# Kernel tuning notes

Hardware: AMD Instinct MI355X
Metric: run time of the kernel (lower is better)

The kernel has to match this reference:

```python
import jax, jax.numpy as jnp
import numpy as np

RES = 192
VOXEL_LEN = 2.0 / (RES - 1)
AABB_LO, AABB_HI = -1.0, 1.0
SH_DIM = 9
UNIFORM = 0.5

_C0 = 0.28209479177387814
_C1 = 0.4886025119029199
_C2 = (1.0925484305920792, -1.0925484305920792, 0.31539156525252005,
       -1.0925484305920792, 0.5462742152960396)

_CORNERS = np.array([[-1, -1, -1], [-1, -1, 1], [-1, 1, -1], [-1, 1, 1],
                     [1, -1, -1], [1, -1, 1], [1, 1, -1], [1, 1, 1]], dtype=np.float32)


def _sh_basis(d):
    # degree-2 real spherical harmonics basis, [B, 9]
    x, y, z = d[..., 0], d[..., 1], d[..., 2]
    return jnp.stack([
        jnp.full_like(x, _C0),
        -_C1 * y, _C1 * z, -_C1 * x,
        _C2[0] * x * y, _C2[1] * y * z,
        _C2[2] * (2.0 * z * z - x * x - y * y),
        _C2[3] * x * z, _C2[4] * (x * x - y * y),
    ], axis=-1)


def _interp_weights(xyz):
    # trilinear weights matching get_interp_weights corner ordering, [..., 8]
    x, y, z = xyz[..., 0], xyz[..., 1], xyz[..., 2]
    return jnp.stack([
        (1 - x) * (1 - y) * (1 - z), (1 - x) * (1 - y) * z,
        (1 - x) * y * (1 - z), (1 - x) * y * z,
        x * (1 - y) * (1 - z), x * (1 - y) * z,
        x * y * (1 - z), x * y * z], axis=-1)


def setup_inputs() -> dict:
    key = jax.random.key(0)
    k1, k2, k3 = jax.random.split(key, 3)
    B = 1024
    # rays originating on a radius-3 sphere, pointing roughly at the aabb center
    rays_o = jax.random.normal(k1, (B, 3), dtype=jnp.float32)
    rays_o = 3.0 * rays_o / jnp.linalg.norm(rays_o, axis=-1, keepdims=True)
    rays_d = -rays_o / 3.0 + 0.08 * jax.random.normal(k2, (B, 3), dtype=jnp.float32)
    rays_d = rays_d / jnp.linalg.norm(rays_d, axis=-1, keepdims=True)
    grid_data = 0.1 * jax.random.normal(k3, (RES ** 3, 3 * SH_DIM + 1), dtype=jnp.float32)
    grid_idx = jnp.arange(RES ** 3, dtype=jnp.int32).reshape(RES, RES, RES)
    return {"rays_o": rays_o, "rays_d": rays_d, "grid_data": grid_data,
            "grid_idx": grid_idx, "n_samples": 400}


def reference(rays_o, rays_d, grid_data, grid_idx, n_samples):
    B = rays_o.shape[0]
    step = VOXEL_LEN
    # --- get_intersections (no-grad in original) ---
    op = (AABB_HI - rays_o) / rays_d
    on = (AABB_LO - rays_o) / rays_d
    t_in = jnp.max(jnp.minimum(op, on), axis=-1)   # [B]
    t_out = jnp.min(jnp.maximum(op, on), axis=-1)  # [B]
    w = jnp.linspace(0.0, 1.0, n_samples, dtype=rays_o.dtype)
    start = t_in + UNIFORM * step
    end = t_in + UNIFORM * step * n_samples
    intrs = start[:, None] * (1.0 - w) + end[:, None] * w   # [B, S]
    intrs = jax.lax.stop_gradient(jnp.minimum(intrs, t_out[:, None]))

    # --- get_intersection_ids: neighbor voxel gather coordinates ---
    pts = rays_o[:, None, :] + intrs[:, :, None] * rays_d[:, None, :]  # [B,S,3]
    offs = jnp.asarray(_CORNERS) * (VOXEL_LEN / 2)                      # [8,3]
    neigh = pts[:, :, None, :] + offs[None, None]                       # [B,S,8,3]
    ngc = jnp.floor(neigh / VOXEL_LEN + 1e-5)
    centers = jnp.clip((ngc + 0.5) * VOXEL_LEN,
                       AABB_LO + VOXEL_LEN / 2, AABB_HI - VOXEL_LEN / 2)
    ids = jnp.clip((ngc + RES / 2).astype(jnp.int32), 0, RES - 1)
    xyzs = (pts - centers[:, :, 0, :]) / VOXEL_LEN                      # [B,S,3]
    nidx = grid_idx[ids[..., 0], ids[..., 1], ids[..., 2]]              # [B,S,8]

    # --- gather + trilinear interpolation (weights are non-diff in original) ---
    nd = grid_data[nidx]                                                 # [B,S,8,28]
    weights = jax.lax.stop_gradient(_interp_weights(xyzs))              # [B,S,8]
    feat = jnp.einsum('bsec,bse->bsc', nd, weights)                      # [B,S,28]

    sigma = feat[..., -1]                                                # [B,S]
    sh = feat[..., :-1].reshape(B, -1, 3, SH_DIM)                        # [B,S,3,9]
    dirs = rays_d / jnp.linalg.norm(rays_d, axis=-1, keepdims=True)
    rgb = jnp.einsum('bsck,bk->bsc', sh, _sh_basis(dirs))                # [B,S,3]

    # --- volumetric_rendering (uses S-1 intervals) ---
    dists = jnp.diff(intrs, axis=1) * jnp.linalg.norm(rays_d, axis=-1, keepdims=True)
    alpha = 1.0 - jnp.exp(-jax.nn.relu(sigma[:, :-1]) * dists)           # [B,S-1]
    cum = jnp.concatenate([jnp.ones((B, 1), alpha.dtype),
                           jnp.cumprod(1.0 - alpha[:, :-1] + 1e-10, axis=-1)], axis=-1)
    abs_light = alpha * cum
    acc = abs_light.sum(-1)
    rgb_map = (abs_light[..., None] * jax.nn.sigmoid(rgb[:, :-1])).sum(axis=1)  # [B,3]
    depth = jax.lax.stop_gradient((abs_light * intrs[:, :-1]).sum(-1))
    rgb_map = rgb_map + (1.0 - acc[:, None])  # white background
    return rgb_map, alpha, depth
```

## Files before the change

kernel.cpp:

```cpp
#include <hip/hip_runtime.h>
#include <cstddef>


constexpr int   RES  = 192;
constexpr float VLEN = 2.0f / 191.0f;
constexpr int   SM1  = 399;
constexpr int   ROWB = 28 * 4;

__global__ __launch_bounds__(512) void nerf_render(
    const float* __restrict__ rays_o,
    const float* __restrict__ rays_d,
    const float* __restrict__ grid_data,
    float* __restrict__ out, int B)
{
  const int b    = blockIdx.x;
  const int tid  = threadIdx.x;
  const int wave = tid >> 6;
  const int lane = tid & 63;
  const int srel = lane >> 3;
  const int r    = lane & 7;

  __shared__ float s_alpha[SM1];
  __shared__ float s_rgb0[SM1];
  __shared__ float s_rgb1[SM1];
  __shared__ float s_rgb2[SM1];
  __shared__ int4  s_m0[SM1];
  __shared__ int4  s_m1[SM1];
  __shared__ float s_m2[SM1];
  __shared__ float s_bs[9];

  const float ox = rays_o[b*3+0], oy = rays_o[b*3+1], oz = rays_o[b*3+2];
  const float dx = rays_d[b*3+0], dy = rays_d[b*3+1], dz = rays_d[b*3+2];

  const float opx = (1.0f - ox)/dx, onx = (-1.0f - ox)/dx;
  const float opy = (1.0f - oy)/dy, ony = (-1.0f - oy)/dy;
  const float opz = (1.0f - oz)/dz, onz = (-1.0f - oz)/dz;
  const float t_in  = fmaxf(fmaxf(fminf(opx,onx), fminf(opy,ony)), fminf(opz,onz));
  const float t_out = fminf(fminf(fmaxf(opx,onx), fmaxf(opy,ony)), fmaxf(opz,onz));
  const float h = 0.5f * VLEN;
  const float dnorm = sqrtf(dx*dx + dy*dy + dz*dz);

  if (tid == 0) {
    const float inv = 1.0f / dnorm;
    const float x = dx*inv, y = dy*inv, z = dz*inv;
    s_bs[0] = 0.28209479177387814f;
    s_bs[1] = -0.4886025119029199f * y;
    s_bs[2] =  0.4886025119029199f * z;
    s_bs[3] = -0.4886025119029199f * x;
    s_bs[4] =  1.0925484305920792f * x*y;
    s_bs[5] = -1.0925484305920792f * y*z;
    s_bs[6] =  0.31539156525252005f * (2.0f*z*z - x*x - y*y);
    s_bs[7] = -1.0925484305920792f * x*z;
    s_bs[8] =  0.5462742152960396f * (x*x - y*y);
  }

  const float hv = 0.5f * VLEN;
  const float inv_vlen = 1.0f / VLEN;

  if (tid < SM1) {
    const int s = tid;
    const float t  = fminf(t_in + h*(float)(s+1), t_out);
    const float px = ox + t*dx, py = oy + t*dy, pz = oz + t*dz;

    const float nx0 = floorf((px - hv)*inv_vlen + 1e-5f);
    const float nx1 = floorf((px + hv)*inv_vlen + 1e-5f);
    const float ny0 = floorf((py - hv)*inv_vlen + 1e-5f);
    const float ny1 = floorf((py + hv)*inv_vlen + 1e-5f);
    const float nz0 = floorf((pz - hv)*inv_vlen + 1e-5f);
    const float nz1 = floorf((pz + hv)*inv_vlen + 1e-5f);

    const int ix0 = min(max((int)(nx0 + 96.0f), 0), RES-1);
    const int ix1 = min(max((int)(nx1 + 96.0f), 0), RES-1);
    const int iy0 = min(max((int)(ny0 + 96.0f), 0), RES-1);
    const int iy1 = min(max((int)(ny1 + 96.0f), 0), RES-1);
    const int iz0 = min(max((int)(nz0 + 96.0f), 0), RES-1);
    const int iz1 = min(max((int)(nz1 + 96.0f), 0), RES-1);

    const float cx = fminf(fmaxf((nx0 + 0.5f)*VLEN, -1.0f + hv), 1.0f - hv);
    const float cy = fminf(fmaxf((ny0 + 0.5f)*VLEN, -1.0f + hv), 1.0f - hv);
    const float cz = fminf(fmaxf((nz0 + 0.5f)*VLEN, -1.0f + hv), 1.0f - hv);
    const float fx = (px - cx)*inv_vlen, fy = (py - cy)*inv_vlen, fz = (pz - cz)*inv_vlen;

    const int x0 = ix0 * (RES*RES*ROWB), x1 = ix1 * (RES*RES*ROWB);
    const int y0 = iy0 * (RES*ROWB),     y1 = iy1 * (RES*ROWB);
    s_m0[s] = make_int4(x0 + y0, x0 + y1, x1 + y0, x1 + y1);
    s_m1[s] = make_int4(iz0 * ROWB, iz1 * ROWB,
                        __float_as_int(fx), __float_as_int(fy));
    s_m2[s] = fz;
  }
  __syncthreads();

  float c0[4], c1[4], c2[4], cs[4];
  #pragma unroll
  for (int j = 0; j < 4; ++j) {
    const int c = 4*r + j;
    float b0 = 0.0f, b1 = 0.0f, b2 = 0.0f, bsg = 0.0f;
    if (c < 9)       b0  = s_bs[c];
    else if (c < 18) b1  = s_bs[c - 9];
    else if (c < 27) b2  = s_bs[c - 18];
    else if (c == 27) bsg = 1.0f;
    c0[j] = b0; c1[j] = b1; c2[j] = b2; cs[j] = bsg;
  }

  float* out_rgb   = out;
  float* out_alpha = out + (size_t)B*3;
  float* out_depth = out + (size_t)B*3 + (size_t)B*SM1;

  const char* gbase = (const char*)grid_data + 16*min(r, 6);

  float4 va[2][8];
  int4   m1s[2];
  float  m2s[2];

  auto issue = [&](int p, int slot) {
    const int sc = min(p*64 + wave*8 + srel, SM1-1);
    const int4 a0 = s_m0[sc];
    const int4 a1 = s_m1[sc];
    m1s[slot] = a1;
    m2s[slot] = s_m2[sc];
    va[slot][0] = *reinterpret_cast<const float4*>(gbase + (a0.x + a1.x));
    va[slot][1] = *reinterpret_cast<const float4*>(gbase + (a0.x + a1.y));
    va[slot][2] = *reinterpret_cast<const float4*>(gbase + (a0.y + a1.x));
    va[slot][3] = *reinterpret_cast<const float4*>(gbase + (a0.y + a1.y));
    va[slot][4] = *reinterpret_cast<const float4*>(gbase + (a0.z + a1.x));
    va[slot][5] = *reinterpret_cast<const float4*>(gbase + (a0.z + a1.y));
    va[slot][6] = *reinterpret_cast<const float4*>(gbase + (a0.w + a1.x));
    va[slot][7] = *reinterpret_cast<const float4*>(gbase + (a0.w + a1.y));
  };

  auto consume = [&](int p, int slot) {
    const int s = p*64 + wave*8 + srel;
    if (s >= SM1) return;
    const float fx = __int_as_float(m1s[slot].z);
    const float fy = __int_as_float(m1s[slot].w);
    const float fz = m2s[slot];
    const float wx0 = 1.0f - fx, wy0 = 1.0f - fy, wz0 = 1.0f - fz;
    const float p00 = wx0*wy0, p01 = wx0*fy, p10 = fx*wy0, p11 = fx*fy;
    const float w[8] = { p00*wz0, p00*fz, p01*wz0, p01*fz,
                         p10*wz0, p10*fz, p11*wz0, p11*fz };
    float ax = 0.f, ay = 0.f, az = 0.f, aw = 0.f;
    #pragma unroll
    for (int e = 0; e < 8; ++e) {
      ax = fmaf(w[e], va[slot][e].x, ax);
      ay = fmaf(w[e], va[slot][e].y, ay);
      az = fmaf(w[e], va[slot][e].z, az);
      aw = fmaf(w[e], va[slot][e].w, aw);
    }
    float pr0 = ax*c0[0] + ay*c0[1] + az*c0[2] + aw*c0[3];
    float pr1 = ax*c1[0] + ay*c1[1] + az*c1[2] + aw*c1[3];
    float pr2 = ax*c2[0] + ay*c2[1] + az*c2[2] + aw*c2[3];
    float sg  = ax*cs[0] + ay*cs[1] + az*cs[2] + aw*cs[3];
    #pragma unroll
    for (int o = 1; o <= 4; o <<= 1) {
      pr0 += __shfl_xor(pr0, o, 64);
      pr1 += __shfl_xor(pr1, o, 64);
      pr2 += __shfl_xor(pr2, o, 64);
      sg  += __shfl_xor(sg,  o, 64);
    }
    if (r == 0) {
      const float t  = fminf(t_in + h*(float)(s+1), t_out);
      const float tn = fminf(t_in + h*(float)(s+2), t_out);
      const float dist = (tn - t) * dnorm;
      const float sig  = fmaxf(sg, 0.0f);
      s_alpha[s] = 1.0f - __expf(-sig * dist);
      s_rgb0[s] = 1.0f/(1.0f + __expf(-pr0));
      s_rgb1[s] = 1.0f/(1.0f + __expf(-pr1));
      s_rgb2[s] = 1.0f/(1.0f + __expf(-pr2));
    }
  };

  issue(0, 0);
  #pragma unroll
  for (int p = 0; p < 7; ++p) {
    if (p < 6) issue(p + 1, (p + 1) & 1);
    consume(p, p & 1);
  }
  __syncthreads();

  if (tid < SM1) out_alpha[(size_t)b*SM1 + tid] = s_alpha[tid];

  if (tid < 64) {
    const int ln = tid;
    const int s0 = ln * 7;
    float pr = 1.0f;
    #pragma unroll
    for (int i = 0; i < 7; ++i) {
      const int si = s0 + i;
      const float tt = (si < SM1) ? (1.0f - s_alpha[si] + 1e-10f) : 1.0f;
      pr *= tt;
    }
    float incl = pr;
    #pragma unroll
    for (int off = 1; off < 64; off <<= 1) {
      const float vv = __shfl_up(incl, off, 64);
      if (ln >= off) incl *= vv;
    }
    float cum = __shfl_up(incl, 1, 64);
    if (ln == 0) cum = 1.0f;

    float acc = 0.0f, r0 = 0.0f, r1 = 0.0f, r2 = 0.0f, dep = 0.0f;
    #pragma unroll
    for (int i = 0; i < 7; ++i) {
      const int si = s0 + i;
      if (si < SM1) {
        const float al = s_alpha[si];
        const float ab = al * cum;
        acc += ab;
        r0 = fmaf(ab, s_rgb0[si], r0);
        r1 = fmaf(ab, s_rgb1[si], r1);
        r2 = fmaf(ab, s_rgb2[si], r2);
        const float ti = fminf(t_in + h*(float)(si+1), t_out);
        dep = fmaf(ab, ti, dep);
        cum *= (1.0f - al + 1e-10f);
      }
    }
    #pragma unroll
    for (int off = 32; off; off >>= 1) {
      acc += __shfl_down(acc, off, 64);
      r0  += __shfl_down(r0,  off, 64);
      r1  += __shfl_down(r1,  off, 64);
      r2  += __shfl_down(r2,  off, 64);
      dep += __shfl_down(dep, off, 64);
    }
    if (ln == 0) {
      const float bg = 1.0f - acc;
      out_rgb[b*3+0] = r0 + bg;
      out_rgb[b*3+1] = r1 + bg;
      out_rgb[b*3+2] = r2 + bg;
      out_depth[b]   = dep;
    }
  }
}

extern "C" void kernel_launch(void* const* d_in, const int* in_sizes, int n_in,
                              void* d_out, int out_size, void* d_ws, size_t ws_size,
                              hipStream_t stream) {
  const float* rays_o    = (const float*)d_in[0];
  const float* rays_d    = (const float*)d_in[1];
  const float* grid_data = (const float*)d_in[2];
  const int B = in_sizes[0] / 3;
  nerf_render<<<dim3(B), dim3(512), 0, stream>>>(
      rays_o, rays_d, grid_data, (float*)d_out, B);
}
```

Before: 33.72 us.

## Halve block size to 256 threads and drop manual double-buffered gather pipeline

Blocks shrink from 512 to 256 threads with launch bounds targeting 5 blocks per CU. The setup and gather loops become strided so each wave handles more samples. The explicit two-slot register prefetch of grid corners is replaced by a plain loop that loads and consumes in the same iteration. The aim is lower register pressure and more resident waves to hide gather latency, at the cost of less software-managed overlap within each wave.

```diff
diff --git a/kernel.cpp b/kernel.cpp
--- a/kernel.cpp
+++ b/kernel.cpp
@@ -7,7 +7,7 @@
 constexpr int   SM1  = 399;
 constexpr int   ROWB = 28 * 4;
 
-__global__ __launch_bounds__(512) void nerf_render(
+__global__ __launch_bounds__(256, 5) void nerf_render(
     const float* __restrict__ rays_o,
     const float* __restrict__ rays_d,
     const float* __restrict__ grid_data,
@@ -57,8 +57,7 @@
   const float hv = 0.5f * VLEN;
   const float inv_vlen = 1.0f / VLEN;
 
-  if (tid < SM1) {
-    const int s = tid;
+  for (int s = tid; s < SM1; s += 256) {
     const float t  = fminf(t_in + h*(float)(s+1), t_out);
     const float px = ox + t*dx, py = oy + t*dy, pz = oz + t*dz;
 
@@ -102,82 +101,73 @@
     c0[j] = b0; c1[j] = b1; c2[j] = b2; cs[j] = bsg;
   }
 
+  const char* gbase = (const char*)grid_data + 16*min(r, 6);
+
+  for (int p = 0; p < 13; ++p) {
+    const int s = p*32 + wave*8 + srel;
+    if (s < SM1) {
+      const int4 a0 = s_m0[s];
+      const int4 a1 = s_m1[s];
+      const float fz = s_m2[s];
+
+      float4 va[8];
+      va[0] = *reinterpret_cast<const float4*>(gbase + (a0.x + a1.x));
+      va[1] = *reinterpret_cast<const float4*>(gbase + (a0.x + a1.y));
+      va[2] = *reinterpret_cast<const float4*>(gbase + (a0.y + a1.x));
+      va[3] = *reinterpret_cast<const float4*>(gbase + (a0.y + a1.y));
+      va[4] = *reinterpret_cast<const float4*>(gbase + (a0.z + a1.x));
+      va[5] = *reinterpret_cast<const float4*>(gbase + (a0.z + a1.y));
+      va[6] = *reinterpret_cast<const float4*>(gbase + (a0.w + a1.x));
+      va[7] = *reinterpret_cast<const float4*>(gbase + (a0.w + a1.y));
+
+      const float fx = __int_as_float(a1.z);
+      const float fy = __int_as_float(a1.w);
+      const float wx0 = 1.0f - fx, wy0 = 1.0f - fy, wz0 = 1.0f - fz;
+      const float p00 = wx0*wy0, p01 = wx0*fy, p10 = fx*wy0, p11 = fx*fy;
+      const float w[8] = { p00*wz0, p00*fz, p01*wz0, p01*fz,
+                           p10*wz0, p10*fz, p11*wz0, p11*fz };
+
+      float ax = 0.f, ay = 0.f, az = 0.f, aw = 0.f;
+      #pragma unroll
+      for (int e = 0; e < 8; ++e) {
+        ax = fmaf(w[e], va[e].x, ax);
+        ay = fmaf(w[e], va[e].y, ay);
+        az = fmaf(w[e], va[e].z, az);
+        aw = fmaf(w[e], va[e].w, aw);
+      }
+      float pr0 = ax*c0[0] + ay*c0[1] + az*c0[2] + aw*c0[3];
+      float pr1 = ax*c1[0] + ay*c1[1] + az*c1[2] + aw*c1[3];
+      float pr2 = ax*c2[0] + ay*c2[1] + az*c2[2] + aw*c2[3];
+      float sg  = ax*cs[0] + ay*cs[1] + az*cs[2] + aw*cs[3];
+
+      #pragma unroll
+      for (int o = 1; o <= 4; o <<= 1) {
+        pr0 += __shfl_xor(pr0, o, 64);
+        pr1 += __shfl_xor(pr1, o, 64);
+        pr2 += __shfl_xor(pr2, o, 64);
+        sg  += __shfl_xor(sg,  o, 64);
+      }
+
+      if (r == 0) {
+        const float t  = fminf(t_in + h*(float)(s+1), t_out);
+        const float tn = fminf(t_in + h*(float)(s+2), t_out);
+        const float dist = (tn - t) * dnorm;
+        const float sig  = fmaxf(sg, 0.0f);
+        s_alpha[s] = 1.0f - __expf(-sig * dist);
+        s_rgb0[s] = 1.0f/(1.0f + __expf(-pr0));
+        s_rgb1[s] = 1.0f/(1.0f + __expf(-pr1));
+        s_rgb2[s] = 1.0f/(1.0f + __expf(-pr2));
+      }
+    }
+  }
+  __syncthreads();
+
   float* out_rgb   = out;
   float* out_alpha = out + (size_t)B*3;
   float* out_depth = out + (size_t)B*3 + (size_t)B*SM1;
 
-  const char* gbase = (const char*)grid_data + 16*min(r, 6);
-
-  float4 va[2][8];
-  int4   m1s[2];
-  float  m2s[2];
-
-  auto issue = [&](int p, int slot) {
-    const int sc = min(p*64 + wave*8 + srel, SM1-1);
-    const int4 a0 = s_m0[sc];
-    const int4 a1 = s_m1[sc];
-    m1s[slot] = a1;
-    m2s[slot] = s_m2[sc];
-    va[slot][0] = *reinterpret_cast<const float4*>(gbase + (a0.x + a1.x));
-    va[slot][1] = *reinterpret_cast<const float4*>(gbase + (a0.x + a1.y));
-    va[slot][2] = *reinterpret_cast<const float4*>(gbase + (a0.y + a1.x));
-    va[slot][3] = *reinterpret_cast<const float4*>(gbase + (a0.y + a1.y));
-    va[slot][4] = *reinterpret_cast<const float4*>(gbase + (a0.z + a1.x));
-    va[slot][5] = *reinterpret_cast<const float4*>(gbase + (a0.z + a1.y));
-    va[slot][6] = *reinterpret_cast<const float4*>(gbase + (a0.w + a1.x));
-    va[slot][7] = *reinterpret_cast<const float4*>(gbase + (a0.w + a1.y));
-  };
-
-  auto consume = [&](int p, int slot) {
-    const int s = p*64 + wave*8 + srel;
-    if (s >= SM1) return;
-    const float fx = __int_as_float(m1s[slot].z);
-    const float fy = __int_as_float(m1s[slot].w);
-    const float fz = m2s[slot];
-    const float wx0 = 1.0f - fx, wy0 = 1.0f - fy, wz0 = 1.0f - fz;
-    const float p00 = wx0*wy0, p01 = wx0*fy, p10 = fx*wy0, p11 = fx*fy;
-    const float w[8] = { p00*wz0, p00*fz, p01*wz0, p01*fz,
-                         p10*wz0, p10*fz, p11*wz0, p11*fz };
-    float ax = 0.f, ay = 0.f, az = 0.f, aw = 0.f;
-    #pragma unroll
-    for (int e = 0; e < 8; ++e) {
-      ax = fmaf(w[e], va[slot][e].x, ax);
-      ay = fmaf(w[e], va[slot][e].y, ay);
-      az = fmaf(w[e], va[slot][e].z, az);
-      aw = fmaf(w[e], va[slot][e].w, aw);
-    }
-    float pr0 = ax*c0[0] + ay*c0[1] + az*c0[2] + aw*c0[3];
-    float pr1 = ax*c1[0] + ay*c1[1] + az*c1[2] + aw*c1[3];
-    float pr2 = ax*c2[0] + ay*c2[1] + az*c2[2] + aw*c2[3];
-    float sg  = ax*cs[0] + ay*cs[1] + az*cs[2] + aw*cs[3];
-    #pragma unroll
-    for (int o = 1; o <= 4; o <<= 1) {
-      pr0 += __shfl_xor(pr0, o, 64);
-      pr1 += __shfl_xor(pr1, o, 64);
-      pr2 += __shfl_xor(pr2, o, 64);
-      sg  += __shfl_xor(sg,  o, 64);
-    }
-    if (r == 0) {
-      const float t  = fminf(t_in + h*(float)(s+1), t_out);
-      const float tn = fminf(t_in + h*(float)(s+2), t_out);
-      const float dist = (tn - t) * dnorm;
-      const float sig  = fmaxf(sg, 0.0f);
-      s_alpha[s] = 1.0f - __expf(-sig * dist);
-      s_rgb0[s] = 1.0f/(1.0f + __expf(-pr0));
-      s_rgb1[s] = 1.0f/(1.0f + __expf(-pr1));
-      s_rgb2[s] = 1.0f/(1.0f + __expf(-pr2));
-    }
-  };
-
-  issue(0, 0);
-  #pragma unroll
-  for (int p = 0; p < 7; ++p) {
-    if (p < 6) issue(p + 1, (p + 1) & 1);
-    consume(p, p & 1);
-  }
-  __syncthreads();
-
-  if (tid < SM1) out_alpha[(size_t)b*SM1 + tid] = s_alpha[tid];
+  for (int s = tid; s < SM1; s += 256)
+    out_alpha[(size_t)b*SM1 + s] = s_alpha[s];
 
   if (tid < 64) {
     const int ln = tid;
@@ -239,6 +229,6 @@
   const float* rays_d    = (const float*)d_in[1];
   const float* grid_data = (const float*)d_in[2];
   const int B = in_sizes[0] / 3;
-  nerf_render<<<dim3(B), dim3(512), 0, stream>>>(
+  nerf_render<<<dim3(B), dim3(256), 0, stream>>>(
       rays_o, rays_d, grid_data, (float*)d_out, B);
 }
```

Result: slower. 34.46 us (+2.2%).
